# Kernel tuning notes

Measured on AMD Instinct MI355X. Metric: run time of the kernel, lower is better.

Reference implementation:

```python
import math
import jax, jax.numpy as jnp
import numpy as np

LAYOUT = (64, 64, 1088, 5184)  # [text_end/startof0, startof0, startof1, endofall]
N_HEAD = 16
HIDDEN = 1024


def _offsets(kH, kW, causal):
    # row-major offsets of a centered kHxkW window; causal keeps the first
    # kH*kW//2+1 entries (all positions at or before the center in raster order)
    offs = [(a - kH // 2, b - kW // 2) for a in range(kH) for b in range(kW)]
    return offs[: kH * kW // 2 + 1] if causal else offs


def _shift(xp, rows0, cols0, di, dj, ph, pw):
    # xp: zero-padded [B,C,Hk+2ph,Wk+2pw]; gather key/value aligned to each query cell
    return xp[:, :, rows0 + di + ph, :][:, :, :, cols0 + dj + pw]


def f_similar(q, k, kH, kW, causal):
    # q: [B,C,Hq,Wq], k: [B,C,Hk,Wk] -> [B,Hq,Wq,K]; out-of-bound keys score 0
    Hq, Wq = q.shape[2], q.shape[3]
    Hk, Wk = k.shape[2], k.shape[3]
    ph, pw = kH // 2, kW // 2
    kp = jnp.pad(k, ((0, 0), (0, 0), (ph, ph), (pw, pw)))
    rows0 = jnp.arange(Hq) // (Hq // Hk)  # query cell -> key-grid center
    cols0 = jnp.arange(Wq) // (Wq // Wk)
    scores = [jnp.einsum('bchw,bchw->bhw', q, _shift(kp, rows0, cols0, di, dj, ph, pw))
              for (di, dj) in _offsets(kH, kW, causal)]
    return jnp.stack(scores, axis=-1)


def f_weighting(v, p, kH, kW, causal):
    # v: [B,C,Hk,Wk], p: [B,Hq,Wq,K] -> [B,C,Hq,Wq]; out-of-bound values are 0
    Hq, Wq = p.shape[1], p.shape[2]
    Hk, Wk = v.shape[2], v.shape[3]
    ph, pw = kH // 2, kW // 2
    vp = jnp.pad(v, ((0, 0), (0, 0), (ph, ph), (pw, pw)))
    rows0 = jnp.arange(Hq) // (Hq // Hk)
    cols0 = jnp.arange(Wq) // (Wq // Wk)
    out = jnp.zeros((v.shape[0], v.shape[1], Hq, Wq), v.dtype)
    for o, (di, dj) in enumerate(_offsets(kH, kW, causal)):
        out = out + p[..., o][:, None] * _shift(vp, rows0, cols0, di, dj, ph, pw)
    return out


def transpose_and_split(x, layout, n_head):
    b, s, h = x.shape
    c = h // n_head
    x = jnp.transpose(x, (0, 2, 1)).reshape(b * n_head, c, s)
    x_text = x[..., :layout[0]]
    s0 = int(math.isqrt(layout[2] - layout[1]))
    s1 = int(math.isqrt(layout[3] - layout[2]))
    x0 = x[..., layout[1]:layout[2]].reshape(b * n_head, c, s0, s0)
    x1 = x[..., layout[2]:layout[3]].reshape(b * n_head, c, s1, s1)
    return x, x_text, x0, x1


def sparse_attention_2d(q, k, v, n_head, layout, mask, ks, ks2):
    b, s, hn = q.shape
    c = hn // n_head
    bn = b * n_head
    t = layout[0]
    n0 = layout[2] - layout[1]
    n1 = layout[3] - layout[2]
    q = q * (1.0 / math.sqrt(c))
    q_all, q_text, q0, q1 = transpose_and_split(q, layout, n_head)
    k_all, k_text, k0, k1 = transpose_and_split(k, layout, n_head)
    v_all, v_text, v0, v1 = transpose_and_split(v, layout, n_head)

    # all queries -> text keys, masked
    m = mask[:, None]  # [b,1,s,t]
    sat = jnp.einsum('bci,bcj->bij', q_all, k_text).reshape(b, n_head, s, t)
    sat = (sat * m - 10000.0 * (1.0 - m)).reshape(bn, s, t)

    s00 = f_similar(q0, k0, ks, ks, True)    # [bn,32,32,ks*ks//2+1]
    s11 = f_similar(q1, k1, ks, ks, True)    # [bn,64,64,ks*ks//2+1]
    s10 = f_similar(q1, k0, ks2, ks2, False) # [bn,64,64,ks2*ks2]
    k00, k10, k11 = s00.shape[-1], s10.shape[-1], s11.shape[-1]

    probs_text = jax.nn.softmax(sat[:, :t], axis=-1)
    probs_0 = jax.nn.softmax(
        jnp.concatenate([sat[:, layout[1]:layout[2]], s00.reshape(bn, n0, k00)], axis=-1), axis=-1)
    probs_1 = jax.nn.softmax(
        jnp.concatenate([sat[:, layout[2]:layout[3]],
                         s10.reshape(bn, n1, k10),
                         s11.reshape(bn, n1, k11)], axis=-1), axis=-1)

    # all -> text context (layout[0]==layout[1] so the pad block is empty)
    probs_a2t = jnp.concatenate([probs_text, probs_0[:, :, :t], probs_1[:, :, :t]], axis=1)
    ctx_text = jnp.einsum('bhij,bhcj->bihc',
                          probs_a2t.reshape(b, n_head, s, t),
                          v_text.reshape(b, n_head, c, t)).reshape(b, s, hn)

    c00 = f_weighting(v0, probs_0[:, :, t:].reshape(s00.shape), ks, ks, True)
    c10 = f_weighting(v0, probs_1[:, :, t:t + k10].reshape(s10.shape), ks2, ks2, False)
    c11 = f_weighting(v1, probs_1[:, :, t + k10:].reshape(s11.shape), ks, ks, True)

    ctx_01 = jnp.concatenate([jnp.zeros((bn, c, layout[1]), q.dtype),
                              c00.reshape(bn, c, n0),
                              (c10 + c11).reshape(bn, c, n1)], axis=-1)
    ctx_01 = jnp.transpose(ctx_01.reshape(b, hn, s), (0, 2, 1))
    return ctx_text + ctx_01


def setup_inputs() -> dict:
    key = jax.random.key(0)
    ks = jax.random.split(key, 3)
    b, s, h, t = 4, LAYOUT[3], HIDDEN, LAYOUT[0]
    return {
        "hidden_states": jax.random.normal(ks[0], (b, s, h), jnp.float32),
        "mask": jnp.ones((b, s, t), jnp.float32),
        "w_qkv": jax.random.normal(ks[1], (h, 3 * h), jnp.float32) * 0.02,
        "b_qkv": jnp.zeros((3 * h,), jnp.float32),
        "w_out": jax.random.normal(ks[2], (h, h), jnp.float32) * 0.02,
        "b_out": jnp.zeros((h,), jnp.float32),
        "kernel_size": 9,
        "kernel_size2": 7,
    }


def reference(hidden_states, mask, w_qkv, b_qkv, w_out, b_out, kernel_size, kernel_size2):
    qkv = hidden_states @ w_qkv + b_qkv
    q, k, v = jnp.split(qkv, 3, axis=-1)
    ctx = sparse_attention_2d(q, k, v, N_HEAD, LAYOUT, mask, kernel_size, kernel_size2)
    return ctx @ w_out + b_out
```

## Files before the change

kernel.cpp:

```cpp
#include <hip/hip_runtime.h>
#include <hip/hip_bf16.h>

#define S_TOT 5184
#define S_PAD 5216
#define T_TXT 64
#define OFF0  64
#define OFF1  1088
#define NHEAD 16
#define CH    64
#define HID   1024
#define BATCH 4
#define BN_TOT (BATCH*NHEAD)
#define MTOT  (BATCH*S_TOT)

typedef __attribute__((ext_vector_type(8))) short bf16x8;
typedef __attribute__((ext_vector_type(8))) _Float16 f16x8;
typedef __attribute__((ext_vector_type(4))) float f32x4;
typedef __attribute__((ext_vector_type(2))) _Float16 h2v;

__device__ __forceinline__ unsigned int f2bf(float x) {
  unsigned int u = __float_as_uint(x);
  unsigned int r = u + 0x7fffu + ((u >> 16) & 1u);
  return r >> 16;
}
__device__ __forceinline__ unsigned short f2h(float x) {
  _Float16 h = (_Float16)x;
  return __builtin_bit_cast(unsigned short, h);
}
__device__ __forceinline__ h2v h2(unsigned int u) { return __builtin_bit_cast(h2v, u); }
__device__ __forceinline__ float fd2(unsigned int a, unsigned int b, float c) {
  return __builtin_amdgcn_fdot2(h2(a), h2(b), c, false);
}
__device__ __forceinline__ unsigned int pklo(unsigned int a, unsigned int b) { return (a & 0xffffu) | (b << 16); }
__device__ __forceinline__ unsigned int pkhi(unsigned int a, unsigned int b) { return (a >> 16) | (b & 0xffff0000u); }
__device__ __forceinline__ f16x8 ld8h(const unsigned short* p) {
  return __builtin_bit_cast(f16x8, *(const uint4*)p);
}

__device__ __forceinline__ void gload_lds16(const short* g, short* l) {
  __builtin_amdgcn_global_load_lds(
      (const __attribute__((address_space(1))) unsigned int*)g,
      (__attribute__((address_space(3))) unsigned int*)l, 16, 0, 0);
}

__global__ __launch_bounds__(256) void cvt_bf16(const float* __restrict__ in,
                                                unsigned int* __restrict__ out, int n8) {
  const int i = blockIdx.x * 256 + threadIdx.x;
  if (i >= n8) return;
  const float4 a = ((const float4*)in)[2 * i];
  const float4 b = ((const float4*)in)[2 * i + 1];
  uint4 r;
  r.x = f2bf(a.x) | (f2bf(a.y) << 16);
  r.y = f2bf(a.z) | (f2bf(a.w) << 16);
  r.z = f2bf(b.x) | (f2bf(b.y) << 16);
  r.w = f2bf(b.z) | (f2bf(b.w) << 16);
  ((uint4*)out)[i] = r;
}

__global__ void cvt_T(const float* __restrict__ in, short* __restrict__ out,
                      const int R, const int Cn) {
  __shared__ float t[32][33];
  const int bx = blockIdx.x * 32, by = blockIdx.y * 32;
  const int tx = threadIdx.x, ty = threadIdx.y;
#pragma unroll
  for (int ph = 0; ph < 4; ++ph)
    t[ty + ph * 8][tx] = in[(size_t)(by + ty + ph * 8) * Cn + bx + tx];
  __syncthreads();
#pragma unroll
  for (int ph = 0; ph < 4; ++ph)
    out[(size_t)(bx + ty + ph * 8) * R + by + tx] = (short)f2bf(t[tx][ty + ph * 8]);
}

__global__ void cvt_Tv(const unsigned short* __restrict__ in, unsigned short* __restrict__ out) {
  __shared__ unsigned short t[32][33];
  const int bh = blockIdx.z;
  const int c0 = blockIdx.x * 32;
  const int s0 = blockIdx.y * 32;
  const int tx = threadIdx.x, ty = threadIdx.y;
  const unsigned short* src = in + (size_t)bh * S_TOT * CH;
  unsigned short* dst = out + (size_t)bh * CH * S_PAD;
#pragma unroll
  for (int ph = 0; ph < 4; ++ph)
    t[ty + ph * 8][tx] = src[(size_t)(s0 + ty + ph * 8) * CH + c0 + tx];
  __syncthreads();
#pragma unroll
  for (int ph = 0; ph < 4; ++ph)
    dst[(size_t)(c0 + ty + ph * 8) * S_PAD + s0 + tx] = t[tx][ty + ph * 8];
}

template<int EPI>
__global__ __launch_bounds__(256) void gemm_mfma(
    const short* __restrict__ A, const short* __restrict__ BT,
    const float* __restrict__ bias, float* __restrict__ C,
    unsigned short* __restrict__ qbuf, unsigned short* __restrict__ kbuf,
    unsigned short* __restrict__ vbuf,
    const int M, const int N, const int K)
{
  __shared__ short As[128 * 32];
  __shared__ short Bs[128 * 32];
  const int tid = threadIdx.x;
  const int w = tid >> 6, l = tid & 63;
  int lin = blockIdx.y * gridDim.x + blockIdx.x;
  const int nwg = gridDim.x * gridDim.y;
  lin = (lin & 7) * (nwg >> 3) + (lin >> 3);
  const int bm = (lin % gridDim.x) * 128;
  const int bn = (lin / gridDim.x) * 128;
  const int wr = w >> 1, wc = w & 1;
  const int lr = l & 15, lk = (l >> 4) * 8;

  const short* aSrc = A + (size_t)(bm + w * 32 + (l >> 2)) * K + (l & 3) * 8;
  const short* bSrc = BT + (size_t)(bn + w * 32 + (l >> 2)) * K + (l & 3) * 8;
  short* aDst = As + w * 32 * 32;
  short* bDst = Bs + w * 32 * 32;

  f32x4 acc[4][4];
#pragma unroll
  for (int m = 0; m < 4; ++m)
#pragma unroll
    for (int n = 0; n < 4; ++n) acc[m][n] = (f32x4){0.f, 0.f, 0.f, 0.f};

  for (int k0 = 0; k0 < K; k0 += 32) {
    gload_lds16(aSrc + k0,            aDst);
    gload_lds16(aSrc + k0 + 16 * K,   aDst + 16 * 32);
    gload_lds16(bSrc + k0,            bDst);
    gload_lds16(bSrc + k0 + 16 * K,   bDst + 16 * 32);
    __syncthreads();
    bf16x8 af[4], bfr[4];
#pragma unroll
    for (int m = 0; m < 4; ++m)
      af[m] = *(const bf16x8*)&As[(wr * 64 + m * 16 + lr) * 32 + lk];
#pragma unroll
    for (int n = 0; n < 4; ++n)
      bfr[n] = *(const bf16x8*)&Bs[(wc * 64 + n * 16 + lr) * 32 + lk];
#pragma unroll
    for (int m = 0; m < 4; ++m)
#pragma unroll
      for (int n = 0; n < 4; ++n)
        acc[m][n] = __builtin_amdgcn_mfma_f32_16x16x32_bf16(af[m], bfr[n], acc[m][n], 0, 0, 0);
    __syncthreads();
  }

#pragma unroll
  for (int m = 0; m < 4; ++m) {
    const int row0 = bm + wr * 64 + m * 16 + (l >> 4) * 4;
#pragma unroll
    for (int n = 0; n < 4; ++n) {
      const int col = bn + wc * 64 + n * 16 + lr;
      const float bv = bias[col];
      if constexpr (EPI == 0) {
#pragma unroll
        for (int i = 0; i < 4; ++i)
          C[(size_t)(row0 + i) * N + col] = acc[m][n][i] + bv;
      } else {
        const int type = col >> 10;
        const int head = (col & 1023) >> 6;
        const int chn  = col & 63;
        unsigned short* dst = (type == 0) ? qbuf : ((type == 1) ? kbuf : vbuf);
        const float sc = (type == 0) ? 0.125f : 1.f;
#pragma unroll
        for (int i = 0; i < 4; ++i) {
          const int row = row0 + i;
          const int b_ = row / S_TOT;
          const int s_ = row - b_ * S_TOT;
          dst[(((size_t)(b_ * NHEAD + head)) * S_TOT + s_) * CH + chn] =
              f2h((acc[m][n][i] + bv) * sc);
        }
      }
    }
  }
}

__global__ __launch_bounds__(256) __attribute__((amdgpu_waves_per_eu(2, 8)))
void attn_img1_mfma(
    const unsigned short* __restrict__ qb, const unsigned short* __restrict__ kb,
    const unsigned short* __restrict__ vtf, const unsigned short* __restrict__ maskT,
    short* __restrict__ ctx)
{
  __shared__ unsigned short ldsP[4][16][168];
  const int tid = threadIdx.x;
  const int w = tid >> 6, l = tid & 63;
  const int lr = l & 15, lg = l >> 4;
  const int swz = (blockIdx.x & 7) * ((BN_TOT * 64) >> 3) + (blockIdx.x >> 3);
  const int bh = swz >> 6;
  const int qi = swz & 63;
  const int qj0 = w * 16;
  const int b_ = bh >> 4, head = bh & 15;
  const int s0 = OFF1 + qi * 64 + qj0;
  const size_t vrowbase = (size_t)bh * CH;
  unsigned short* myP = &ldsP[w][0][0];

  const unsigned short* qrow = qb + ((size_t)bh * S_TOT + s0 + lr) * CH + lg * 8;
  const f16x8 aq0 = ld8h(qrow);
  const f16x8 aq1 = ld8h(qrow + 32);

  float m[4], lsum[4];
  f32x4 acc[4];
#pragma unroll
  for (int i = 0; i < 4; ++i) { m[i] = -1e30f; lsum[i] = 0.f; }
#pragma unroll
  for (int n = 0; n < 4; ++n) acc[n] = (f32x4){0.f, 0.f, 0.f, 0.f};

  {
    f32x4 sC[4];
    const unsigned short* kb0 = kb + ((size_t)bh * S_TOT) * CH + lg * 8;
#pragma unroll
    for (int kt = 0; kt < 4; ++kt) {
      const unsigned short* krow = kb0 + (kt * 16 + lr) * CH;
      f32x4 a = (f32x4){0.f, 0.f, 0.f, 0.f};
      a = __builtin_amdgcn_mfma_f32_16x16x32_f16(aq0, ld8h(krow), a, 0, 0, 0);
      a = __builtin_amdgcn_mfma_f32_16x16x32_f16(aq1, ld8h(krow + 32), a, 0, 0, 0);
      sC[kt] = a;
    }
#pragma unroll
    for (int kt = 0; kt < 4; ++kt) {
      const unsigned short* mrow = maskT + (size_t)(kt * 16 + lr) * MTOT + (size_t)b_ * S_TOT + s0 + lg * 4;
#pragma unroll
      for (int i = 0; i < 4; ++i) {
        const float mv = __uint_as_float(((unsigned int)mrow[i]) << 16);
        sC[kt][i] = sC[kt][i] * mv - 10000.f * (1.f - mv);
      }
    }
    float rsc[4], la[4];
#pragma unroll
    for (int i = 0; i < 4; ++i) {
      float mx = fmaxf(fmaxf(sC[0][i], sC[1][i]), fmaxf(sC[2][i], sC[3][i]));
      mx = fmaxf(mx, __shfl_xor(mx, 1));
      mx = fmaxf(mx, __shfl_xor(mx, 2));
      mx = fmaxf(mx, __shfl_xor(mx, 4));
      mx = fmaxf(mx, __shfl_xor(mx, 8));
      const float mn = fmaxf(m[i], mx);
      rsc[i] = __expf(m[i] - mn);
      m[i] = mn;
      la[i] = 0.f;
    }
#pragma unroll
    for (int kt = 0; kt < 4; ++kt)
#pragma unroll
      for (int i = 0; i < 4; ++i) {
        const float p = __expf(sC[kt][i] - m[i]);
        la[i] += p;
        myP[(lg * 4 + i) * 168 + kt * 16 + lr] = f2h(p);
      }
#pragma unroll
    for (int i = 0; i < 4; ++i) {
      float li = la[i];
      li += __shfl_xor(li, 1);
      li += __shfl_xor(li, 2);
      li += __shfl_xor(li, 4);
      li += __shfl_xor(li, 8);
      lsum[i] = lsum[i] * rsc[i] + li;
#pragma unroll
      for (int n = 0; n < 4; ++n) acc[n][i] *= rsc[i];
    }
#pragma unroll
    for (int kt = 0; kt < 2; ++kt) {
      const f16x8 ap = __builtin_bit_cast(f16x8, *(const uint4*)&myP[lr * 168 + kt * 32 + lg * 8]);
      const int sbase = kt * 32 + lg * 8;
#pragma unroll
      for (int n = 0; n < 4; ++n) {
        const f16x8 bv = ld8h(vtf + (vrowbase + n * 16 + lr) * S_PAD + sbase);
        acc[n] = __builtin_amdgcn_mfma_f32_16x16x32_f16(ap, bv, acc[n], 0, 0, 0);
      }
    }
  }

  {
    const int ki0 = qi >> 1, cb = (qj0 >> 1) - 3;
    f32x4 sA[7];
#pragma unroll
    for (int rr = 0; rr < 7; ++rr) sA[rr] = (f32x4){-1e30f, -1e30f, -1e30f, -1e30f};
    const unsigned short* kbA = kb + ((size_t)bh * S_TOT + OFF0) * CH + lg * 8;
    const int kjc = min(max(cb + lr, 0), 31);
#pragma unroll
    for (int rr = 0; rr < 7; ++rr) {
      const int ki = ki0 + rr - 3;
      if ((unsigned)ki < 32u) {
        const unsigned short* krow = kbA + (ki * 32 + kjc) * CH;
        f32x4 a = (f32x4){0.f, 0.f, 0.f, 0.f};
        a = __builtin_amdgcn_mfma_f32_16x16x32_f16(aq0, ld8h(krow), a, 0, 0, 0);
        a = __builtin_amdgcn_mfma_f32_16x16x32_f16(aq1, ld8h(krow + 32), a, 0, 0, 0);
        sA[rr] = a;
      }
    }
    const int kjA = cb + lr;
    float pmax[4] = {-1e30f, -1e30f, -1e30f, -1e30f};
#pragma unroll
    for (int rr = 0; rr < 7; ++rr) {
      const int ki = ki0 + rr - 3;
      const bool rv = (unsigned)ki < 32u;
#pragma unroll
      for (int i = 0; i < 4; ++i) {
        const int kjq = (qj0 + lg * 4 + i) >> 1;
        const int dj = kjA - kjq;
        const bool ok = rv && dj >= -3 && dj <= 3 && kjA >= 0 && kjA < 32;
        sA[rr][i] = ok ? sA[rr][i] : -1e30f;
        pmax[i] = fmaxf(pmax[i], sA[rr][i]);
      }
    }
    float rsc[4], la[4];
#pragma unroll
    for (int i = 0; i < 4; ++i) {
      float mx = pmax[i];
      mx = fmaxf(mx, __shfl_xor(mx, 1));
      mx = fmaxf(mx, __shfl_xor(mx, 2));
      mx = fmaxf(mx, __shfl_xor(mx, 4));
      mx = fmaxf(mx, __shfl_xor(mx, 8));
      const float mn = fmaxf(m[i], mx);
      rsc[i] = __expf(m[i] - mn);
      m[i] = mn;
      la[i] = 0.f;
    }
#pragma unroll
    for (int rr = 0; rr < 7; ++rr)
#pragma unroll
      for (int i = 0; i < 4; ++i) {
        const float p = __expf(sA[rr][i] - m[i]);
        la[i] += p;
        myP[(lg * 4 + i) * 168 + rr * 16 + lr] = f2h(p);
      }
#pragma unroll
    for (int j2 = 0; j2 < 4; ++j2)
      myP[lr * 168 + 112 + lg * 4 + j2] = 0;
#pragma unroll
    for (int i = 0; i < 4; ++i) {
      float li = la[i];
      li += __shfl_xor(li, 1);
      li += __shfl_xor(li, 2);
      li += __shfl_xor(li, 4);
      li += __shfl_xor(li, 8);
      lsum[i] = lsum[i] * rsc[i] + li;
#pragma unroll
      for (int n = 0; n < 4; ++n) acc[n][i] *= rsc[i];
    }
#pragma unroll
    for (int kt = 0; kt < 4; ++kt) {
      const f16x8 ap = __builtin_bit_cast(f16x8, *(const uint4*)&myP[lr * 168 + kt * 32 + lg * 8]);
      const int rowidx = 2 * kt + (lg >> 1);
      const int kiv = min(max(ki0 + rowidx - 3, 0), 31);
      const int sbase = OFF0 + kiv * 32 + cb + (lg & 1) * 8;
#pragma unroll
      for (int n = 0; n < 4; ++n) {
        const f16x8 bv = ld8h(vtf + (vrowbase + n * 16 + lr) * S_PAD + sbase);
        acc[n] = __builtin_amdgcn_mfma_f32_16x16x32_f16(ap, bv, acc[n], 0, 0, 0);
      }
    }
  }

  {
    const int cbB = qj0 - 4;
    f32x4 sB[10];
#pragma unroll
    for (int rr = 0; rr < 10; ++rr) sB[rr] = (f32x4){-1e30f, -1e30f, -1e30f, -1e30f};
    const unsigned short* kbB = kb + ((size_t)bh * S_TOT + OFF1) * CH + lg * 8;
#pragma unroll
    for (int rr = 0; rr < 5; ++rr) {
      const int ki = qi + rr - 4;
      if (ki >= 0) {
#pragma unroll
        for (int t = 0; t < 2; ++t) {
          const int kjc = min(max(cbB + t * 16 + lr, 0), 63);
          const unsigned short* krow = kbB + (ki * 64 + kjc) * CH;
          f32x4 a = (f32x4){0.f, 0.f, 0.f, 0.f};
          a = __builtin_amdgcn_mfma_f32_16x16x32_f16(aq0, ld8h(krow), a, 0, 0, 0);
          a = __builtin_amdgcn_mfma_f32_16x16x32_f16(aq1, ld8h(krow + 32), a, 0, 0, 0);
          sB[rr * 2 + t] = a;
        }
      }
    }
    float pmax[4] = {-1e30f, -1e30f, -1e30f, -1e30f};
#pragma unroll
    for (int rr = 0; rr < 5; ++rr) {
      const int djmax = (rr == 4) ? 0 : 4;
#pragma unroll
      for (int t = 0; t < 2; ++t) {
        const int kj = cbB + t * 16 + lr;
#pragma unroll
        for (int i = 0; i < 4; ++i) {
          const int qj = qj0 + lg * 4 + i;
          const int dj = kj - qj;
          const bool ok = dj >= -4 && dj <= djmax && kj >= 0 && kj < 64;
          sB[rr * 2 + t][i] = ok ? sB[rr * 2 + t][i] : -1e30f;
          pmax[i] = fmaxf(pmax[i], sB[rr * 2 + t][i]);
        }
      }
    }
    float rsc[4], la[4];
#pragma unroll
    for (int i = 0; i < 4; ++i) {
      float mx = pmax[i];
      mx = fmaxf(mx, __shfl_xor(mx, 1));
      mx = fmaxf(mx, __shfl_xor(mx, 2));
      mx = fmaxf(mx, __shfl_xor(mx, 4));
      mx = fmaxf(mx, __shfl_xor(mx, 8));
      const float mn = fmaxf(m[i], mx);
      rsc[i] = __expf(m[i] - mn);
      m[i] = mn;
      la[i] = 0.f;
    }
#pragma unroll
    for (int rr = 0; rr < 5; ++rr)
#pragma unroll
      for (int t = 0; t < 2; ++t)
#pragma unroll
        for (int i = 0; i < 4; ++i) {
          const float p = __expf(sB[rr * 2 + t][i] - m[i]);
          la[i] += p;
          myP[(lg * 4 + i) * 168 + rr * 32 + t * 16 + lr] = f2h(p);
        }
#pragma unroll
    for (int i = 0; i < 4; ++i) {
      float li = la[i];
      li += __shfl_xor(li, 1);
      li += __shfl_xor(li, 2);
      li += __shfl_xor(li, 4);
      li += __shfl_xor(li, 8);
      lsum[i] = lsum[i] * rsc[i] + li;
#pragma unroll
      for (int n = 0; n < 4; ++n) acc[n][i] *= rsc[i];
    }
#pragma unroll
    for (int kt = 0; kt < 5; ++kt) {
      const f16x8 ap = __builtin_bit_cast(f16x8, *(const uint4*)&myP[lr * 168 + kt * 32 + lg * 8]);
      const int kiv = max(qi + kt - 4, 0);
      const int sbase = OFF1 + kiv * 64 + cbB + lg * 8;
#pragma unroll
      for (int n = 0; n < 4; ++n) {
        const f16x8 bv = ld8h(vtf + (vrowbase + n * 16 + lr) * S_PAD + sbase);
        acc[n] = __builtin_amdgcn_mfma_f32_16x16x32_f16(ap, bv, acc[n], 0, 0, 0);
      }
    }
  }

  const int ki0f = qi >> 1;
#pragma unroll
  for (int i = 0; i < 4; ++i) {
    const int qj = qj0 + lg * 4 + i;
    const int kjq = qj >> 1;
    const int nInvA = max(0, 3 - ki0f) + max(0, ki0f - 28);
    const int oobA  = max(0, 3 - kjq) + max(0, kjq - 28);
    const int nInvB = max(0, 4 - qi);
    const int oobB  = max(0, 4 - qj) + max(0, qj - 59);
    const int cnt = nInvA * 7 + (7 - nInvA) * oobA
                  + nInvB * 9 + (4 - nInvB) * oobB + max(0, 4 - qj);
    const float lf = lsum[i] + (float)cnt * __expf(-m[i]);
    const float inv = 1.f / lf;
    short* cp = ctx + ((size_t)(b_ * S_TOT) + s0 + lg * 4 + i) * HID + head * CH;
#pragma unroll
    for (int n = 0; n < 4; ++n)
      cp[n * 16 + lr] = (short)f2bf(acc[n][i] * inv);
  }
}

__global__ __launch_bounds__(128) __attribute__((amdgpu_waves_per_eu(2, 8)))
void attn_img0_mfma(
    const unsigned short* __restrict__ qb, const unsigned short* __restrict__ kb,
    const unsigned short* __restrict__ vtf, const unsigned short* __restrict__ maskT,
    short* __restrict__ ctx)
{
  __shared__ unsigned short ldsP[2][16][168];
  const int tid = threadIdx.x;
  const int w = tid >> 6, l = tid & 63;
  const int lr = l & 15, lg = l >> 4;
  const int swz = (blockIdx.x & 7) * ((BN_TOT * 32) >> 3) + (blockIdx.x >> 3);
  const int bh = swz >> 5;
  const int qi = swz & 31;
  const int qj0 = w * 16;
  const int b_ = bh >> 4, head = bh & 15;
  const int s0 = OFF0 + qi * 32 + qj0;
  const size_t vrowbase = (size_t)bh * CH;
  unsigned short* myP = &ldsP[w][0][0];

  const unsigned short* qrow = qb + ((size_t)bh * S_TOT + s0 + lr) * CH + lg * 8;
  const f16x8 aq0 = ld8h(qrow);
  const f16x8 aq1 = ld8h(qrow + 32);

  f32x4 sC[4];
  {
    const unsigned short* kb0 = kb + ((size_t)bh * S_TOT) * CH + lg * 8;
#pragma unroll
    for (int kt = 0; kt < 4; ++kt) {
      const unsigned short* krow = kb0 + (kt * 16 + lr) * CH;
      f32x4 a = (f32x4){0.f, 0.f, 0.f, 0.f};
      a = __builtin_amdgcn_mfma_f32_16x16x32_f16(aq0, ld8h(krow), a, 0, 0, 0);
      a = __builtin_amdgcn_mfma_f32_16x16x32_f16(aq1, ld8h(krow + 32), a, 0, 0, 0);
      sC[kt] = a;
    }
  }
  const int cbB = qj0 - 4;
  f32x4 sB[10];
  {
#pragma unroll
    for (int rr = 0; rr < 10; ++rr) sB[rr] = (f32x4){-1e30f, -1e30f, -1e30f, -1e30f};
    const unsigned short* kbB = kb + ((size_t)bh * S_TOT + OFF0) * CH + lg * 8;
#pragma unroll
    for (int rr = 0; rr < 5; ++rr) {
      const int ki = qi + rr - 4;
      if (ki >= 0) {
#pragma unroll
        for (int t = 0; t < 2; ++t) {
          const int kjc = min(max(cbB + t * 16 + lr, 0), 31);
          const unsigned short* krow = kbB + (ki * 32 + kjc) * CH;
          f32x4 a = (f32x4){0.f, 0.f, 0.f, 0.f};
          a = __builtin_amdgcn_mfma_f32_16x16x32_f16(aq0, ld8h(krow), a, 0, 0, 0);
          a = __builtin_amdgcn_mfma_f32_16x16x32_f16(aq1, ld8h(krow + 32), a, 0, 0, 0);
          sB[rr * 2 + t] = a;
        }
      }
    }
  }

#pragma unroll
  for (int kt = 0; kt < 4; ++kt) {
    const unsigned short* mrow = maskT + (size_t)(kt * 16 + lr) * MTOT + (size_t)b_ * S_TOT + s0 + lg * 4;
#pragma unroll
    for (int i = 0; i < 4; ++i) {
      const float mv = __uint_as_float(((unsigned int)mrow[i]) << 16);
      sC[kt][i] = sC[kt][i] * mv - 10000.f * (1.f - mv);
    }
  }
#pragma unroll
  for (int rr = 0; rr < 5; ++rr) {
    const int djmax = (rr == 4) ? 0 : 4;
#pragma unroll
    for (int t = 0; t < 2; ++t) {
      const int kj = cbB + t * 16 + lr;
#pragma unroll
      for (int i = 0; i < 4; ++i) {
        const int qj = qj0 + lg * 4 + i;
        const int dj = kj - qj;
        const bool ok = dj >= -4 && dj <= djmax && kj >= 0 && kj < 32;
        sB[rr * 2 + t][i] = ok ? sB[rr * 2 + t][i] : -1e30f;
      }
    }
  }

  float m[4], lsum[4];
#pragma unroll
  for (int i = 0; i < 4; ++i) {
    float mx = fmaxf(fmaxf(sC[0][i], sC[1][i]), fmaxf(sC[2][i], sC[3][i]));
#pragma unroll
    for (int rr = 0; rr < 10; ++rr) mx = fmaxf(mx, sB[rr][i]);
    mx = fmaxf(mx, __shfl_xor(mx, 1));
    mx = fmaxf(mx, __shfl_xor(mx, 2));
    mx = fmaxf(mx, __shfl_xor(mx, 4));
    mx = fmaxf(mx, __shfl_xor(mx, 8));
    m[i] = mx;
    float li = 0.f;
#pragma unroll
    for (int kt = 0; kt < 4; ++kt) { const float p = __expf(sC[kt][i] - mx); sC[kt][i] = p; li += p; }
#pragma unroll
    for (int rr = 0; rr < 10; ++rr) { const float p = __expf(sB[rr][i] - mx); sB[rr][i] = p; li += p; }
    li += __shfl_xor(li, 1);
    li += __shfl_xor(li, 2);
    li += __shfl_xor(li, 4);
    li += __shfl_xor(li, 8);
    lsum[i] = li;
  }

  f32x4 acc[4];
#pragma unroll
  for (int n = 0; n < 4; ++n) acc[n] = (f32x4){0.f, 0.f, 0.f, 0.f};

  {
#pragma unroll
    for (int kt = 0; kt < 4; ++kt)
#pragma unroll
      for (int i = 0; i < 4; ++i)
        myP[(lg * 4 + i) * 168 + kt * 16 + lr] = f2h(sC[kt][i]);
#pragma unroll
    for (int kt = 0; kt < 2; ++kt) {
      const f16x8 ap = __builtin_bit_cast(f16x8, *(const uint4*)&myP[lr * 168 + kt * 32 + lg * 8]);
      const int sbase = kt * 32 + lg * 8;
#pragma unroll
      for (int n = 0; n < 4; ++n) {
        const f16x8 bv = ld8h(vtf + (vrowbase + n * 16 + lr) * S_PAD + sbase);
        acc[n] = __builtin_amdgcn_mfma_f32_16x16x32_f16(ap, bv, acc[n], 0, 0, 0);
      }
    }
  }
  {
#pragma unroll
    for (int rr = 0; rr < 5; ++rr)
#pragma unroll
      for (int t = 0; t < 2; ++t)
#pragma unroll
        for (int i = 0; i < 4; ++i)
          myP[(lg * 4 + i) * 168 + rr * 32 + t * 16 + lr] = f2h(sB[rr * 2 + t][i]);
#pragma unroll
    for (int kt = 0; kt < 5; ++kt) {
      const f16x8 ap = __builtin_bit_cast(f16x8, *(const uint4*)&myP[lr * 168 + kt * 32 + lg * 8]);
      const int kiv = max(qi + kt - 4, 0);
      const int sbase = OFF0 + kiv * 32 + cbB + lg * 8;
#pragma unroll
      for (int n = 0; n < 4; ++n) {
        const f16x8 bv = ld8h(vtf + (vrowbase + n * 16 + lr) * S_PAD + sbase);
        acc[n] = __builtin_amdgcn_mfma_f32_16x16x32_f16(ap, bv, acc[n], 0, 0, 0);
      }
    }
  }

#pragma unroll
  for (int i = 0; i < 4; ++i) {
    const int qj = qj0 + lg * 4 + i;
    const int nInvB = max(0, 4 - qi);
    const int oobB  = max(0, 4 - qj) + max(0, qj - 27);
    const int cnt = nInvB * 9 + (4 - nInvB) * oobB + max(0, 4 - qj);
    const float lf = lsum[i] + (float)cnt * __expf(-m[i]);
    const float inv = 1.f / lf;
    short* cp = ctx + ((size_t)(b_ * S_TOT) + s0 + lg * 4 + i) * HID + head * CH;
#pragma unroll
    for (int n = 0; n < 4; ++n)
      cp[n * 16 + lr] = (short)f2bf(acc[n][i] * inv);
  }
}

__device__ __forceinline__ float dot8h(const uint4 qd, const unsigned short* __restrict__ kp) {
  const uint4 a = *(const uint4*)kp;
  float s = 0.f;
  s = fd2(a.x, qd.x, s); s = fd2(a.y, qd.y, s);
  s = fd2(a.z, qd.z, s); s = fd2(a.w, qd.w, s);
  return s;
}
__device__ __forceinline__ void pv2d(float& a0, float& a1, unsigned int dA, unsigned int dB, h2v pp) {
  a0 = __builtin_amdgcn_fdot2(h2(pklo(dA, dB)), pp, a0, false);
  a1 = __builtin_amdgcn_fdot2(h2(pkhi(dA, dB)), pp, a1, false);
}
__device__ __forceinline__ void pv2q(float* __restrict__ acc, uint4 A, uint4 B, h2v pp) {
  pv2d(acc[0], acc[1], A.x, B.x, pp);
  pv2d(acc[2], acc[3], A.y, B.y, pp);
  pv2d(acc[4], acc[5], A.z, B.z, pp);
  pv2d(acc[6], acc[7], A.w, B.w, pp);
}

template<int W, bool MASKED>
__device__ __forceinline__ void row_upd(const uint4 qd,
                                        const unsigned short* __restrict__ krow,
                                        const unsigned short* __restrict__ vrow,
                                        const int kj0, const int limit,
                                        const unsigned short* __restrict__ maskT,
                                        const int rowIdx,
                                        float& m, float& l, float* __restrict__ acc, int& cnt) {
  float s[W];
#pragma unroll
  for (int j = 0; j < W; ++j) {
    const int kj = kj0 + j;
    const bool ok = (unsigned)kj < (unsigned)limit;
    float d = dot8h(qd, krow + (ok ? kj : 0) * CH);
    d += __shfl_xor(d, 1);
    d += __shfl_xor(d, 2);
    d += __shfl_xor(d, 4);
    if constexpr (MASKED) {
      const float mv = __uint_as_float(((unsigned int)maskT[(size_t)kj * MTOT + rowIdx]) << 16);
      s[j] = d * mv - 10000.f * (1.f - mv);
    } else {
      s[j] = ok ? d : -1e30f;
      cnt += ok ? 0 : 1;
    }
  }
  float smax = s[0];
#pragma unroll
  for (int j = 1; j < W; ++j) smax = fmaxf(smax, s[j]);
  const float mn = fmaxf(m, smax);
  const float r = __expf(m - mn);
  m = mn;
  l *= r;
#pragma unroll
  for (int i = 0; i < 8; ++i) acc[i] *= r;
  float p[W];
#pragma unroll
  for (int j = 0; j < W; ++j) { p[j] = __expf(s[j] - mn); l += p[j]; }
#pragma unroll
  for (int j = 0; j < W; j += 2) {
    const int kja = kj0 + j;
    const bool oka = (unsigned)kja < (unsigned)limit;
    const uint4 A = *(const uint4*)(vrow + (oka ? kja : 0) * CH);
    uint4 B; float pb;
    if (j + 1 < W) {
      const int kjb = kja + 1;
      const bool okb = (unsigned)kjb < (unsigned)limit;
      B = *(const uint4*)(vrow + (okb ? kjb : 0) * CH);
      pb = p[j + 1];
    } else {
      B = A; pb = 0.f;
    }
    const h2v pp = __builtin_bit_cast(h2v, __builtin_amdgcn_cvt_pkrtz(p[j], pb));
    pv2q(acc, A, B, pp);
  }
}

__device__ __forceinline__ void store_q8(short* ctx, size_t base,
                                         const float* acc, float inv) {
  unsigned int* cp = (unsigned int*)(ctx + base);
#pragma unroll
  for (int i = 0; i < 4; ++i)
    cp[i] = f2bf(acc[2 * i] * inv) | (f2bf(acc[2 * i + 1] * inv) << 16);
}

__global__ __launch_bounds__(256) __attribute__((amdgpu_waves_per_eu(4, 8)))
void attn_text(
    const unsigned short* __restrict__ qb, const unsigned short* __restrict__ kb,
    const unsigned short* __restrict__ vb, const unsigned short* __restrict__ maskT,
    short* __restrict__ ctx)
{
  const int t = blockIdx.x * 256 + threadIdx.x;
  const int oct = t & 7;
  const int qidx = t >> 3;
  const int bh = qidx >> 6;
  const int tq = qidx & 63;
  const int b_ = bh >> 4, head = bh & 15;

  const uint4 qd = *(const uint4*)(qb + ((size_t)bh * S_TOT + tq) * CH + oct * 8);

  float m = -1e30f, l = 0.f;
  float acc[8];
#pragma unroll
  for (int i = 0; i < 8; ++i) acc[i] = 0.f;
  int cnt = 0;

  const unsigned short* kt = kb + (size_t)bh * S_TOT * CH + oct * 8;
  const unsigned short* vt = vb + (size_t)bh * S_TOT * CH + oct * 8;
  const int rowIdx = b_ * S_TOT + tq;
  for (int t8 = 0; t8 < 8; ++t8)
    row_upd<8, true>(qd, kt, vt, t8 * 8, T_TXT, maskT, rowIdx, m, l, acc, cnt);
  store_q8(ctx, ((size_t)rowIdx) * HID + head * CH + oct * 8, acc, 1.f / l);
}

extern "C" void kernel_launch(void* const* d_in, const int* in_sizes, int n_in,
                              void* d_out, int out_size, void* d_ws, size_t ws_size,
                              hipStream_t stream) {
  const float* hidden = (const float*)d_in[0];
  const float* mask   = (const float*)d_in[1];
  const float* w_qkv  = (const float*)d_in[2];
  const float* b_qkv  = (const float*)d_in[3];
  const float* w_out  = (const float*)d_in[4];
  const float* b_out  = (const float*)d_in[5];
  float* out = (float*)d_out;

  const size_t NB = (size_t)BN_TOT * S_TOT * CH;
  unsigned short* qbuf = (unsigned short*)d_ws;
  unsigned short* kbuf = qbuf + NB;
  unsigned short* vbuf = kbuf + NB;
  short* hbf   = (short*)(vbuf + NB);
  short* wqkvT = hbf + NB;
  short* woutT = wqkvT + (size_t)3072 * 1024;
  short* maskT = woutT + (size_t)1024 * 1024;
  unsigned short* vtf = (unsigned short*)(maskT + (size_t)T_TXT * MTOT);

  cvt_bf16<<<(int)((NB / 8 + 255) / 256), 256, 0, stream>>>(hidden, (unsigned int*)hbf, (int)(NB / 8));
  cvt_T<<<dim3(3072 / 32, 1024 / 32), dim3(32, 8), 0, stream>>>(w_qkv, wqkvT, 1024, 3072);
  cvt_T<<<dim3(1024 / 32, 1024 / 32), dim3(32, 8), 0, stream>>>(w_out, woutT, 1024, 1024);
  cvt_T<<<dim3(T_TXT / 32, MTOT / 32), dim3(32, 8), 0, stream>>>(mask, maskT, MTOT, T_TXT);

  gemm_mfma<1><<<dim3(MTOT / 128, 3072 / 128), 256, 0, stream>>>(
      hbf, wqkvT, b_qkv, nullptr, qbuf, kbuf, vbuf, MTOT, 3072, 1024);

  cvt_Tv<<<dim3(CH / 32, S_TOT / 32, BN_TOT), dim3(32, 8), 0, stream>>>(vbuf, vtf);

  short* ctx = hbf;
  attn_text<<<(BN_TOT * T_TXT * 8) / 256, 256, 0, stream>>>(qbuf, kbuf, vbuf, (unsigned short*)maskT, ctx);
  attn_img0_mfma<<<BN_TOT * 32, 128, 0, stream>>>(qbuf, kbuf, vtf, (unsigned short*)maskT, ctx);
  attn_img1_mfma<<<BN_TOT * 64, 256, 0, stream>>>(qbuf, kbuf, vtf, (unsigned short*)maskT, ctx);

  gemm_mfma<0><<<dim3(MTOT / 128, 1024 / 128), 256, 0, stream>>>(
      ctx, woutT, b_out, out, nullptr, nullptr, nullptr, MTOT, 1024, 1024);
}
```

Baseline: 543.6 us.

## Rewrite GEMM as 256x256 tile with double-buffered swizzled LDS pipeline

Replaces the 128x128, 256-thread GEMM with a 256x256-tile, 512-thread kernel using a K-step of 64. Global-to-LDS loads go into two buffers with an XOR swizzle, and the next tiles are prefetched while MFMAs run, with s_setprio raised around the MFMA blocks. The workgroup remap is also generalized to handle counts not divisible by 8. This targets the QKV and output projection GEMMs: more operand reuse per load, fewer LDS bank conflicts, and overlap of memory with compute. In exchange it uses 128KB of LDS and many more accumulator registers, and it launches far fewer workgroups (81x4 for the output GEMM).

```diff
diff --git a/kernel.cpp b/kernel.cpp
--- a/kernel.cpp
+++ b/kernel.cpp
@@ -89,63 +89,121 @@
 }
 
 template<int EPI>
-__global__ __launch_bounds__(256) void gemm_mfma(
+__global__ __launch_bounds__(512) __attribute__((amdgpu_waves_per_eu(2)))
+void gemm_mfma256(
     const short* __restrict__ A, const short* __restrict__ BT,
     const float* __restrict__ bias, float* __restrict__ C,
     unsigned short* __restrict__ qbuf, unsigned short* __restrict__ kbuf,
     unsigned short* __restrict__ vbuf,
     const int M, const int N, const int K)
 {
-  __shared__ short As[128 * 32];
-  __shared__ short Bs[128 * 32];
+  __shared__ short SH[65536];
   const int tid = threadIdx.x;
   const int w = tid >> 6, l = tid & 63;
-  int lin = blockIdx.y * gridDim.x + blockIdx.x;
-  const int nwg = gridDim.x * gridDim.y;
-  lin = (lin & 7) * (nwg >> 3) + (lin >> 3);
-  const int bm = (lin % gridDim.x) * 128;
-  const int bn = (lin / gridDim.x) * 128;
-  const int wr = w >> 1, wc = w & 1;
-  const int lr = l & 15, lk = (l >> 4) * 8;
-
-  const short* aSrc = A + (size_t)(bm + w * 32 + (l >> 2)) * K + (l & 3) * 8;
-  const short* bSrc = BT + (size_t)(bn + w * 32 + (l >> 2)) * K + (l & 3) * 8;
-  short* aDst = As + w * 32 * 32;
-  short* bDst = Bs + w * 32 * 32;
-
-  f32x4 acc[4][4];
-#pragma unroll
-  for (int m = 0; m < 4; ++m)
+  const int wm = w >> 2, wn = w & 3;
+  const int lr = l & 15, lg = l >> 4;
+
+  int lin;
+  {
+    const int orig = blockIdx.y * gridDim.x + blockIdx.x;
+    const int nwg = gridDim.x * gridDim.y;
+    const int q = nwg >> 3, r = nwg & 7;
+    const int x = orig & 7, idx = orig >> 3;
+    lin = (x < r ? x * (q + 1) : r * (q + 1) + (x - r) * q) + idx;
+  }
+  const int bm = (lin % gridDim.x) * 256;
+  const int bn = (lin / gridDim.x) * 256;
+
+  auto stageA = [&](int tt, int h) {
+    const int kb = tt * 64;
+    const int lo = ((tt & 1) * 2 + h) * 8192;
+#pragma unroll
+    for (int c = 0; c < 2; ++c) {
+      const int idx = c * 512 + tid;
+      const int row = idx >> 3;
+      const int col = ((idx & 7) ^ (row & 7)) * 8;
+      gload_lds16(A + (size_t)(bm + h * 128 + row) * K + kb + col, SH + lo + idx * 8);
+    }
+  };
+  auto stageB = [&](int tt, int h) {
+    const int kb = tt * 64;
+    const int lo = 32768 + ((tt & 1) * 2 + h) * 8192;
+#pragma unroll
+    for (int c = 0; c < 2; ++c) {
+      const int idx = c * 512 + tid;
+      const int row = idx >> 3;
+      const int col = ((idx & 7) ^ (row & 7)) * 8;
+      gload_lds16(BT + (size_t)(bn + h * 128 + row) * K + kb + col, SH + lo + idx * 8);
+    }
+  };
+
+  f32x4 acc[8][4];
+#pragma unroll
+  for (int m = 0; m < 8; ++m)
 #pragma unroll
     for (int n = 0; n < 4; ++n) acc[m][n] = (f32x4){0.f, 0.f, 0.f, 0.f};
 
-  for (int k0 = 0; k0 < K; k0 += 32) {
-    gload_lds16(aSrc + k0,            aDst);
-    gload_lds16(aSrc + k0 + 16 * K,   aDst + 16 * 32);
-    gload_lds16(bSrc + k0,            bDst);
-    gload_lds16(bSrc + k0 + 16 * K,   bDst + 16 * 32);
-    __syncthreads();
-    bf16x8 af[4], bfr[4];
-#pragma unroll
-    for (int m = 0; m < 4; ++m)
-      af[m] = *(const bf16x8*)&As[(wr * 64 + m * 16 + lr) * 32 + lk];
+  const int NT = K >> 6;
+  stageA(0, 0); stageA(0, 1); stageB(0, 0); stageB(0, 1);
+  stageA(1, 0); stageA(1, 1); stageB(1, 0); stageB(1, 1);
+  asm volatile("s_waitcnt vmcnt(8)" ::: "memory");
+  __builtin_amdgcn_s_barrier();
+  __builtin_amdgcn_sched_barrier(0);
+
+  const int aoffBase = wm * 8192;
+  const int boffBase = 32768 + (wn >> 1) * 8192 + (wn & 1) * 64 * 64;
+  const int sw = (lr & 7) << 3;
+
+  for (int t = 0; t < NT; ++t) {
+    const int b = t & 1;
+    const int ao = b * 16384 + aoffBase;
+    const int bo = boffBase + b * 16384;
+    bf16x8 af[8], bfr[4];
+#pragma unroll
+    for (int m = 0; m < 8; ++m)
+      af[m] = *(const bf16x8*)&SH[ao + (m * 16 + lr) * 64 + ((lg * 8) ^ sw)];
 #pragma unroll
     for (int n = 0; n < 4; ++n)
-      bfr[n] = *(const bf16x8*)&Bs[(wc * 64 + n * 16 + lr) * 32 + lk];
-#pragma unroll
-    for (int m = 0; m < 4; ++m)
+      bfr[n] = *(const bf16x8*)&SH[bo + (n * 16 + lr) * 64 + ((lg * 8) ^ sw)];
+    __builtin_amdgcn_s_setprio(1);
+#pragma unroll
+    for (int m = 0; m < 8; ++m)
 #pragma unroll
       for (int n = 0; n < 4; ++n)
         acc[m][n] = __builtin_amdgcn_mfma_f32_16x16x32_bf16(af[m], bfr[n], acc[m][n], 0, 0, 0);
-    __syncthreads();
-  }
-
-#pragma unroll
-  for (int m = 0; m < 4; ++m) {
-    const int row0 = bm + wr * 64 + m * 16 + (l >> 4) * 4;
+    __builtin_amdgcn_s_setprio(0);
+#pragma unroll
+    for (int m = 0; m < 8; ++m)
+      af[m] = *(const bf16x8*)&SH[ao + (m * 16 + lr) * 64 + ((32 + lg * 8) ^ sw)];
+#pragma unroll
+    for (int n = 0; n < 4; ++n)
+      bfr[n] = *(const bf16x8*)&SH[bo + (n * 16 + lr) * 64 + ((32 + lg * 8) ^ sw)];
+    asm volatile("s_waitcnt lgkmcnt(0)" ::: "memory");
+    __builtin_amdgcn_sched_barrier(0);
+    __builtin_amdgcn_s_barrier();
+    __builtin_amdgcn_sched_barrier(0);
+    if (t + 2 < NT) {
+      stageA(t + 2, 0); stageA(t + 2, 1); stageB(t + 2, 0); stageB(t + 2, 1);
+    }
+    __builtin_amdgcn_s_setprio(1);
+#pragma unroll
+    for (int m = 0; m < 8; ++m)
+#pragma unroll
+      for (int n = 0; n < 4; ++n)
+        acc[m][n] = __builtin_amdgcn_mfma_f32_16x16x32_bf16(af[m], bfr[n], acc[m][n], 0, 0, 0);
+    __builtin_amdgcn_s_setprio(0);
+    if (t + 2 < NT) asm volatile("s_waitcnt vmcnt(8)" ::: "memory");
+    else            asm volatile("s_waitcnt vmcnt(0)" ::: "memory");
+    __builtin_amdgcn_s_barrier();
+    __builtin_amdgcn_sched_barrier(0);
+  }
+
+#pragma unroll
+  for (int m = 0; m < 8; ++m) {
+    const int row0 = bm + wm * 128 + m * 16 + lg * 4;
 #pragma unroll
     for (int n = 0; n < 4; ++n) {
-      const int col = bn + wc * 64 + n * 16 + lr;
+      const int col = bn + wn * 64 + n * 16 + lr;
       const float bv = bias[col];
       if constexpr (EPI == 0) {
 #pragma unroll
@@ -751,7 +809,7 @@
   cvt_T<<<dim3(1024 / 32, 1024 / 32), dim3(32, 8), 0, stream>>>(w_out, woutT, 1024, 1024);
   cvt_T<<<dim3(T_TXT / 32, MTOT / 32), dim3(32, 8), 0, stream>>>(mask, maskT, MTOT, T_TXT);
 
-  gemm_mfma<1><<<dim3(MTOT / 128, 3072 / 128), 256, 0, stream>>>(
+  gemm_mfma256<1><<<dim3(MTOT / 256, 3072 / 256), 512, 0, stream>>>(
       hbf, wqkvT, b_qkv, nullptr, qbuf, kbuf, vbuf, MTOT, 3072, 1024);
 
   cvt_Tv<<<dim3(CH / 32, S_TOT / 32, BN_TOT), dim3(32, 8), 0, stream>>>(vbuf, vtf);
@@ -761,6 +819,6 @@
   attn_img0_mfma<<<BN_TOT * 32, 128, 0, stream>>>(qbuf, kbuf, vtf, (unsigned short*)maskT, ctx);
   attn_img1_mfma<<<BN_TOT * 64, 256, 0, stream>>>(qbuf, kbuf, vtf, (unsigned short*)maskT, ctx);
 
-  gemm_mfma<0><<<dim3(MTOT / 128, 1024 / 128), 256, 0, stream>>>(
+  gemm_mfma256<0><<<dim3(MTOT / 256, 1024 / 256), 512, 0, stream>>>(
       ctx, woutT, b_out, out, nullptr, nullptr, nullptr, MTOT, 1024, 1024);
 }
```

After: 486.3 us. -10.5%, faster.
